# Optimization experiments

Measured on AMD Instinct MI355X. Metric: run time of the kernel, lower is better.

## Reference

```python
import jax, jax.numpy as jnp
import numpy as np

N_NODES = 50000
N_EDGES = 800000
IN_FEAT = 128
HIDDEN = 128
NUM_CLASS = 40


def setup_inputs() -> dict:
    key = jax.random.key(0)
    ks = jax.random.split(key, 8)
    feat = jax.random.normal(ks[0], (N_NODES, IN_FEAT), dtype=jnp.float32)
    # Glorot-ish init scale for reference weights
    W1 = jax.random.normal(ks[1], (IN_FEAT, HIDDEN), dtype=jnp.float32) / np.sqrt(IN_FEAT)
    b1 = jnp.zeros((HIDDEN,), dtype=jnp.float32)
    W2 = jax.random.normal(ks[2], (HIDDEN, HIDDEN), dtype=jnp.float32) / np.sqrt(HIDDEN)
    b2 = jnp.zeros((HIDDEN,), dtype=jnp.float32)
    W3 = jax.random.normal(ks[3], (HIDDEN, NUM_CLASS), dtype=jnp.float32) / np.sqrt(HIDDEN)
    b3 = jnp.zeros((NUM_CLASS,), dtype=jnp.float32)
    src = jax.random.randint(ks[4], (N_EDGES,), 0, N_NODES, dtype=jnp.int32)
    dst = jax.random.randint(ks[5], (N_EDGES,), 0, N_NODES, dtype=jnp.int32)
    return {"feat": feat, "W1": W1, "b1": b1, "W2": W2, "b2": b2,
            "W3": W3, "b3": b3, "src": src, "dst": dst}


def reference(feat, W1, b1, W2, b2, W3, b3, src, dst):
    # symmetric 'both' normalization as in DGL GraphConv:
    # h_dst = deg_in(dst)^{-1/2} * sum_{e:(s->d)} deg_out(s)^{-1/2} * (x_s W) + b
    ones = jnp.ones((src.shape[0],), dtype=feat.dtype)
    out_deg = jax.ops.segment_sum(ones, src, num_segments=N_NODES)
    in_deg = jax.ops.segment_sum(ones, dst, num_segments=N_NODES)
    out_norm = jax.lax.rsqrt(jnp.maximum(out_deg, 1.0))  # [N]
    in_norm = jax.lax.rsqrt(jnp.maximum(in_deg, 1.0))    # [N]

    def gconv(h, W, b):
        h = (h * out_norm[:, None]) @ W                  # [N, d_out]
        agg = jax.ops.segment_sum(h[src], dst, num_segments=N_NODES)
        return agg * in_norm[:, None] + b

    # eval mode: BatchNorm disabled (identity), dropout is a no-op
    h = jax.nn.relu(gconv(feat, W1, b1))
    h = jax.nn.relu(gconv(h, W2, b2))
    return gconv(h, W3, b3)
```

## Files before the change

### kernel.cpp

```cpp
#include <hip/hip_runtime.h>
#include <hip/hip_bf16.h>

#define N_NODES 50000
#define N_EDGES 800000
#define FEAT    128
#define HID     128
#define NCLS    40
#define XPAD    50048

#define RANGE   12500
#define NRANGE  4
#define NS      32
#define SLICE   (N_EDGES / NS)
#define NBLK    49

static constexpr size_t ALIGNB = 256;
static constexpr size_t aln(size_t x){ return (x + ALIGNB - 1) & ~(ALIGNB - 1); }
static constexpr size_t OFF_ONORM   = 0;
static constexpr size_t OFF_INORM   = OFF_ONORM + aln((size_t)N_NODES * 4);
static constexpr size_t OFF_ROWPTR  = OFF_INORM + aln((size_t)N_NODES * 4);
static constexpr size_t OFF_BSUM    = OFF_ROWPTR + aln((size_t)(N_NODES + 1) * 4);
static constexpr size_t OFF_BOFF    = OFF_BSUM + aln(64 * 4);
static constexpr size_t OFF_WT1     = OFF_BOFF + aln(64 * 4);
static constexpr size_t OFF_WT2     = OFF_WT1 + aln((size_t)128 * 128 * 2);
static constexpr size_t OFF_WT3     = OFF_WT2 + aln((size_t)128 * 128 * 2);
static constexpr size_t OFF_ESRC    = OFF_WT3 + aln((size_t)64 * 128 * 2);
static constexpr size_t OFF_HTMP    = OFF_ESRC + aln((size_t)N_EDGES * 4);
static constexpr size_t OFF_XBUF    = OFF_HTMP + aln((size_t)XPAD * 128 * 2);
static constexpr size_t OFF_PART    = OFF_HTMP;

__device__ __forceinline__ float bflo(unsigned u){
  union { unsigned i; float f; } c; c.i = u << 16; return c.f;
}
__device__ __forceinline__ float bfhi(unsigned u){
  union { unsigned i; float f; } c; c.i = u & 0xffff0000u; return c.f;
}
__device__ __forceinline__ unsigned pkbf(float a, float b){
  union { __hip_bfloat16 h; unsigned short u; } ca, cb;
  ca.h = __float2bfloat16(a); cb.h = __float2bfloat16(b);
  return ((unsigned)cb.u << 16) | (unsigned)ca.u;
}
__device__ __forceinline__ unsigned short bf1(float a){
  union { __hip_bfloat16 h; unsigned short u; } c;
  c.h = __float2bfloat16(a); return c.u;
}

typedef __attribute__((ext_vector_type(8))) short bf16x8;
typedef __attribute__((ext_vector_type(4))) float f32x4;

__global__ void k_prep_all(const float* __restrict__ W1, const float* __restrict__ W2,
                           const float* __restrict__ W3,
                           unsigned* __restrict__ wt1, unsigned* __restrict__ wt2,
                           unsigned* __restrict__ wt3){
  int b = blockIdx.x, t = threadIdx.x;
  const float* W; unsigned* Wt; int WC; int idx;
  if (b < 32)      { W = W1; Wt = wt1; WC = 128; idx = b * 256 + t; }
  else if (b < 64) { W = W2; Wt = wt2; WC = 128; idx = (b - 32) * 256 + t; }
  else             { W = W3; Wt = wt3; WC = 40;  idx = (b - 64) * 256 + t; }
  int c = idx >> 6, kp = idx & 63;
  float v0 = (c < WC) ? W[(size_t)(2 * kp)     * WC + c] : 0.f;
  float v1 = (c < WC) ? W[(size_t)(2 * kp + 1) * WC + c] : 0.f;
  Wt[idx] = pkbf(v0, v1);
}

__global__ __launch_bounds__(1024) void k_hist_lds(const int* __restrict__ src,
                                                   const int* __restrict__ dst,
                                                   unsigned* __restrict__ part){
  __shared__ unsigned h[RANGE];
  const int s = blockIdx.x, r = blockIdx.y, z = blockIdx.z;
  const int* __restrict__ idx = z ? src : dst;
  const int lo = r * RANGE;
  for (int i = threadIdx.x; i < RANGE; i += 1024) h[i] = 0;
  __syncthreads();
  const int e0 = s * SLICE;
  for (int e = e0 + threadIdx.x; e < e0 + SLICE; e += 1024){
    int v = idx[e] - lo;
    if ((unsigned)v < RANGE) atomicAdd(&h[v], 1u);
  }
  __syncthreads();
  unsigned* p = part + (((size_t)z * NRANGE + r) * NS + s) * RANGE;
  for (int i = threadIdx.x; i < RANGE; i += 1024) p[i] = h[i];
}

__global__ __launch_bounds__(1024) void k_scan1(const unsigned* __restrict__ part,
                                                int* __restrict__ rowptr,
                                                unsigned* __restrict__ bsum,
                                                float* __restrict__ inorm,
                                                float* __restrict__ onorm){
  __shared__ int wsum[16];
  const int t = threadIdx.x, lane = t & 63, w = t >> 6;
  const int i = blockIdx.x * 1024 + t;
  int v = 0;
  if (i < N_NODES){
    int r = i / RANGE, off = i % RANGE;
    const unsigned* pi = part + ((size_t)r * NS) * RANGE + off;
    const unsigned* po = part + (((size_t)NRANGE + r) * NS) * RANGE + off;
    unsigned si = 0, so = 0;
    #pragma unroll 8
    for (int s = 0; s < NS; ++s){
      si += pi[(size_t)s * RANGE];
      so += po[(size_t)s * RANGE];
    }
    inorm[i] = rsqrtf(fmaxf((float)si, 1.0f));
    onorm[i] = rsqrtf(fmaxf((float)so, 1.0f));
    v = (int)si;
  }
  int x = v;
  #pragma unroll
  for (int off = 1; off < 64; off <<= 1){
    int y = __shfl_up(x, off, 64);
    if (lane >= off) x += y;
  }
  if (lane == 63) wsum[w] = x;
  __syncthreads();
  if (w == 0 && lane < 16){
    int s = wsum[lane];
    #pragma unroll
    for (int off = 1; off < 16; off <<= 1){
      int y = __shfl_up(s, off, 64);
      if (lane >= off) s += y;
    }
    wsum[lane] = s;
  }
  __syncthreads();
  int woff = (w > 0) ? wsum[w - 1] : 0;
  if (i < N_NODES) rowptr[i] = woff + x - v;
  if (t == 0) bsum[blockIdx.x] = (unsigned)wsum[15];
}

__global__ void k_scan2(const unsigned* __restrict__ bsum, unsigned* __restrict__ boff){
  const int t = threadIdx.x;
  int v = (t < NBLK) ? (int)bsum[t] : 0;
  int x = v;
  #pragma unroll
  for (int off = 1; off < 64; off <<= 1){
    int y = __shfl_up(x, off, 64);
    if (t >= off) x += y;
  }
  if (t < NBLK) boff[t] = (unsigned)(x - v);
  if (t == NBLK - 1) boff[NBLK] = (unsigned)x;
}

__global__ __launch_bounds__(1024) void k_scan3(int* __restrict__ rowptr,
                                                const unsigned* __restrict__ boff,
                                                unsigned* __restrict__ part){
  const int i = blockIdx.x * 1024 + threadIdx.x;
  if (i < N_NODES){
    int rp = rowptr[i] + (int)boff[blockIdx.x];
    rowptr[i] = rp;
    int r = i / RANGE, off = i % RANGE;
    unsigned* p = part + ((size_t)r * NS) * RANGE + off;
    unsigned run = (unsigned)rp;
    #pragma unroll 8
    for (int s = 0; s < NS; ++s){
      unsigned c = p[(size_t)s * RANGE];
      p[(size_t)s * RANGE] = run;
      run += c;
    }
  } else if (i == N_NODES) rowptr[i] = (int)boff[NBLK];
}

__global__ __launch_bounds__(1024) void k_scatter_lds(const int* __restrict__ src,
                                                      const int* __restrict__ dst,
                                                      const unsigned* __restrict__ part,
                                                      int* __restrict__ esrc){
  __shared__ unsigned cur[RANGE];
  const int s = blockIdx.x, r = blockIdx.y;
  const int lo = r * RANGE;
  const unsigned* p = part + ((size_t)r * NS + s) * RANGE;
  for (int i = threadIdx.x; i < RANGE; i += 1024) cur[i] = p[i];
  __syncthreads();
  const int e0 = s * SLICE;
  for (int e = e0 + threadIdx.x; e < e0 + SLICE; e += 1024){
    int v = dst[e] - lo;
    if ((unsigned)v < RANGE){
      unsigned pos = atomicAdd(&cur[v], 1u);
      esrc[pos] = src[e];
    }
  }
}

template<int CT, int WCOUT, int OUTC, bool IN_F32>
__global__ __launch_bounds__(256) void k_gemm_mfma(const void* __restrict__ xin,
                                                   const unsigned short* __restrict__ wt,
                                                   const float* __restrict__ onorm,
                                                   unsigned short* __restrict__ outb){
  __shared__ unsigned short Wl[CT * 16][136];
  const int t = threadIdx.x;
  const int lane = t & 63;
  const int w = t >> 6;
  const int ln15 = lane & 15;
  const int quad = lane >> 4;

  {
    const uint4* w4 = (const uint4*)wt;
    #pragma unroll
    for (int i = 0; i < CT; ++i){
      int idx = t + i * 256;
      int row = idx >> 4, q = idx & 15;
      *(uint4*)&Wl[row][q * 8] = w4[idx];
    }
  }
  __syncthreads();

  f32x4 acc[CT];
  #pragma unroll
  for (int ct = 0; ct < CT; ++ct) acc[ct] = (f32x4){0.f, 0.f, 0.f, 0.f};

  const int xr = min(blockIdx.x * 64 + w * 16 + ln15, N_NODES - 1);
  #pragma unroll
  for (int kp = 0; kp < 4; ++kp){
    bf16x8 a;
    if (IN_F32){
      const float4* x4 = (const float4*)xin + (size_t)xr * 32;
      float4 p0 = x4[kp * 8 + quad * 2];
      float4 p1 = x4[kp * 8 + quad * 2 + 1];
      union { bf16x8 v; unsigned u[4]; } ua;
      ua.u[0] = pkbf(p0.x, p0.y); ua.u[1] = pkbf(p0.z, p0.w);
      ua.u[2] = pkbf(p1.x, p1.y); ua.u[3] = pkbf(p1.z, p1.w);
      a = ua.v;
    } else {
      const unsigned short* xrow = (const unsigned short*)xin + (size_t)xr * 128;
      a = *(const bf16x8*)(xrow + kp * 32 + quad * 8);
    }
    #pragma unroll
    for (int ct = 0; ct < CT; ++ct){
      bf16x8 b = *(const bf16x8*)&Wl[ct * 16 + ln15][kp * 32 + quad * 8];
      acc[ct] = __builtin_amdgcn_mfma_f32_16x16x32_bf16(a, b, acc[ct], 0, 0, 0);
    }
  }

  const int rowbase = blockIdx.x * 64 + w * 16 + quad * 4;
  float o[4];
  #pragma unroll
  for (int j = 0; j < 4; ++j){
    int r = rowbase + j;
    o[j] = (r < N_NODES) ? onorm[r] : 0.f;
  }
  #pragma unroll
  for (int ct = 0; ct < CT; ++ct){
    int col = ct * 16 + ln15;
    if (WCOUT < CT * 16 && col >= WCOUT) continue;
    #pragma unroll
    for (int j = 0; j < 4; ++j){
      int r = rowbase + j;
      if (r < N_NODES)
        outb[(size_t)r * OUTC + col] = bf1(acc[ct][j] * o[j]);
    }
  }
}

template<int CW, bool RELU, bool OUTBF>
__global__ __launch_bounds__(256) void k_agg(const unsigned* __restrict__ htmp,
                                             const int* __restrict__ rowptr,
                                             const int* __restrict__ esrc,
                                             const float* __restrict__ inorm,
                                             const float* __restrict__ bias,
                                             void* __restrict__ outv){
  constexpr int CU = CW / 2;
  const int wave = threadIdx.x >> 6;
  const int lane = threadIdx.x & 63;
  const int node = blockIdx.x * 4 + wave;
  if (node >= N_NODES) return;
  const int start = rowptr[node], end = rowptr[node + 1];
  float aL[4] = {0.f, 0.f, 0.f, 0.f};
  float aH[4] = {0.f, 0.f, 0.f, 0.f};
  for (int e0 = start; e0 < end; e0 += 64){
    const int n = min(64, end - e0);
    int el = (lane < n) ? esrc[e0 + lane] : 0;
    int j = 0;
    for (; j + 8 <= n; j += 8){
      int ss[8];
      #pragma unroll
      for (int q = 0; q < 8; ++q) ss[q] = __shfl(el, j + q);
      if (lane < CU){
        unsigned uu[8];
        #pragma unroll
        for (int q = 0; q < 8; ++q) uu[q] = htmp[(size_t)ss[q] * CU + lane];
        #pragma unroll
        for (int q = 0; q < 8; ++q){ aL[q & 3] += bflo(uu[q]); aH[q & 3] += bfhi(uu[q]); }
      }
    }
    for (; j + 4 <= n; j += 4){
      int ss[4];
      #pragma unroll
      for (int q = 0; q < 4; ++q) ss[q] = __shfl(el, j + q);
      if (lane < CU){
        unsigned uu[4];
        #pragma unroll
        for (int q = 0; q < 4; ++q) uu[q] = htmp[(size_t)ss[q] * CU + lane];
        #pragma unroll
        for (int q = 0; q < 4; ++q){ aL[q] += bflo(uu[q]); aH[q] += bfhi(uu[q]); }
      }
    }
    for (; j < n; ++j){
      int s0 = __shfl(el, j);
      if (lane < CU){
        unsigned u0 = htmp[(size_t)s0 * CU + lane];
        aL[0] += bflo(u0); aH[0] += bfhi(u0);
      }
    }
  }
  if (lane < CU){
    float sc = inorm[node];
    float y0 = ((aL[0] + aL[1]) + (aL[2] + aL[3])) * sc + bias[2 * lane];
    float y1 = ((aH[0] + aH[1]) + (aH[2] + aH[3])) * sc + bias[2 * lane + 1];
    if (RELU){ y0 = fmaxf(y0, 0.f); y1 = fmaxf(y1, 0.f); }
    if (OUTBF){
      ((unsigned*)outv)[(size_t)node * CU + lane] = pkbf(y0, y1);
    } else {
      float2 v; v.x = y0; v.y = y1;
      *(float2*)&((float*)outv)[(size_t)node * CW + 2 * lane] = v;
    }
  }
}

extern "C" void kernel_launch(void* const* d_in, const int* in_sizes, int n_in,
                              void* d_out, int out_size, void* d_ws, size_t ws_size,
                              hipStream_t stream){
  const float* feat = (const float*)d_in[0];
  const float* W1   = (const float*)d_in[1];
  const float* b1   = (const float*)d_in[2];
  const float* W2   = (const float*)d_in[3];
  const float* b2   = (const float*)d_in[4];
  const float* W3   = (const float*)d_in[5];
  const float* b3   = (const float*)d_in[6];
  const int* src = (const int*)d_in[7];
  const int* dst = (const int*)d_in[8];
  float* out = (float*)d_out;

  char* ws = (char*)d_ws;
  float*    onorm   = (float*)   (ws + OFF_ONORM);
  float*    inorm   = (float*)   (ws + OFF_INORM);
  int*      rowptr  = (int*)     (ws + OFF_ROWPTR);
  unsigned* bsum    = (unsigned*)(ws + OFF_BSUM);
  unsigned* boff    = (unsigned*)(ws + OFF_BOFF);
  unsigned* wt1     = (unsigned*)(ws + OFF_WT1);
  unsigned* wt2     = (unsigned*)(ws + OFF_WT2);
  unsigned* wt3     = (unsigned*)(ws + OFF_WT3);
  int*      esrc    = (int*)     (ws + OFF_ESRC);
  unsigned short* htmp = (unsigned short*)(ws + OFF_HTMP);
  unsigned short* xbuf = (unsigned short*)(ws + OFF_XBUF);
  unsigned* part    = (unsigned*)(ws + OFF_PART);

  k_prep_all    <<<80, 256, 0, stream>>>(W1, W2, W3, wt1, wt2, wt3);
  k_hist_lds    <<<dim3(NS, NRANGE, 2), 1024, 0, stream>>>(src, dst, part);
  k_scan1       <<<NBLK, 1024, 0, stream>>>(part, rowptr, bsum, inorm, onorm);
  k_scan2       <<<1, 64, 0, stream>>>(bsum, boff);
  k_scan3       <<<NBLK, 1024, 0, stream>>>(rowptr, boff, part);
  k_scatter_lds <<<dim3(NS, NRANGE), 1024, 0, stream>>>(src, dst, part, esrc);

  const int GB = XPAD / 64;
  const int AB = (N_NODES + 3) / 4;
  k_gemm_mfma<8, 128, 128, true ><<<GB, 256, 0, stream>>>(feat, (unsigned short*)wt1, onorm, htmp);
  k_agg<128, true, true ><<<AB, 256, 0, stream>>>((unsigned*)htmp, rowptr, esrc, inorm, b1, xbuf);
  k_gemm_mfma<8, 128, 128, false><<<GB, 256, 0, stream>>>(xbuf, (unsigned short*)wt2, onorm, htmp);
  k_agg<128, true, true ><<<AB, 256, 0, stream>>>((unsigned*)htmp, rowptr, esrc, inorm, b2, xbuf);
  k_gemm_mfma<4, 40, 40, false><<<GB, 256, 0, stream>>>(xbuf, (unsigned short*)wt3, onorm, htmp);
  k_agg<40, false, false><<<AB, 256, 0, stream>>>((unsigned*)htmp, rowptr, esrc, inorm, b3, out);
}
```

Baseline: 248.7 us.

## Fuse aggregation with following GEMM via LDS tile and fold weight prep into histogram

Layers 1 and 2 aggregation are fused with the next layer's MFMA GEMM. Each 512-thread block gathers 128 node rows, applies norm, bias and ReLU, and stages them as bf16 in LDS before multiplying by the next weight matrix. This removes the round trip of the intermediate xbuf through global memory and two kernel launches. The weight transpose/prep kernel is merged into the histogram kernel to save another launch. The cost is fewer blocks, since only 391 fused blocks run the irregular gather, and extra buffers to avoid aliasing.

New measurement: 267.3 us. 1.07x slower.

```diff
diff --git a/kernel.cpp b/kernel.cpp
--- a/kernel.cpp
+++ b/kernel.cpp
@@ -25,9 +25,10 @@
 static constexpr size_t OFF_WT2     = OFF_WT1 + aln((size_t)128 * 128 * 2);
 static constexpr size_t OFF_WT3     = OFF_WT2 + aln((size_t)128 * 128 * 2);
 static constexpr size_t OFF_ESRC    = OFF_WT3 + aln((size_t)64 * 128 * 2);
-static constexpr size_t OFF_HTMP    = OFF_ESRC + aln((size_t)N_EDGES * 4);
-static constexpr size_t OFF_XBUF    = OFF_HTMP + aln((size_t)XPAD * 128 * 2);
-static constexpr size_t OFF_PART    = OFF_HTMP;
+static constexpr size_t OFF_HTMPA   = OFF_ESRC + aln((size_t)N_EDGES * 4);
+static constexpr size_t OFF_HTMPB   = OFF_HTMPA + aln((size_t)XPAD * 128 * 2);
+static constexpr size_t OFF_HTMPC   = OFF_HTMPB + aln((size_t)XPAD * 128 * 2);
+static constexpr size_t OFF_PART    = OFF_HTMPA;
 
 __device__ __forceinline__ float bflo(unsigned u){
   union { unsigned i; float f; } c; c.i = u << 16; return c.f;
@@ -48,33 +49,35 @@
 typedef __attribute__((ext_vector_type(8))) short bf16x8;
 typedef __attribute__((ext_vector_type(4))) float f32x4;
 
-__global__ void k_prep_all(const float* __restrict__ W1, const float* __restrict__ W2,
-                           const float* __restrict__ W3,
-                           unsigned* __restrict__ wt1, unsigned* __restrict__ wt2,
-                           unsigned* __restrict__ wt3){
-  int b = blockIdx.x, t = threadIdx.x;
-  const float* W; unsigned* Wt; int WC; int idx;
-  if (b < 32)      { W = W1; Wt = wt1; WC = 128; idx = b * 256 + t; }
-  else if (b < 64) { W = W2; Wt = wt2; WC = 128; idx = (b - 32) * 256 + t; }
-  else             { W = W3; Wt = wt3; WC = 40;  idx = (b - 64) * 256 + t; }
-  int c = idx >> 6, kp = idx & 63;
-  float v0 = (c < WC) ? W[(size_t)(2 * kp)     * WC + c] : 0.f;
-  float v1 = (c < WC) ? W[(size_t)(2 * kp + 1) * WC + c] : 0.f;
-  Wt[idx] = pkbf(v0, v1);
-}
-
 __global__ __launch_bounds__(1024) void k_hist_lds(const int* __restrict__ src,
                                                    const int* __restrict__ dst,
-                                                   unsigned* __restrict__ part){
+                                                   unsigned* __restrict__ part,
+                                                   const float* __restrict__ W1,
+                                                   const float* __restrict__ W2,
+                                                   const float* __restrict__ W3,
+                                                   unsigned* __restrict__ wt1,
+                                                   unsigned* __restrict__ wt2,
+                                                   unsigned* __restrict__ wt3){
   __shared__ unsigned h[RANGE];
   const int s = blockIdx.x, r = blockIdx.y, z = blockIdx.z;
-  const int* __restrict__ idx = z ? src : dst;
+  if (z == 0 && r == 0 && s < 20){
+    int idx = s * 1024 + threadIdx.x;
+    const float* W; unsigned* Wt; int WC;
+    if (idx < 8192)       { W = W1; Wt = wt1; WC = 128; }
+    else if (idx < 16384) { W = W2; Wt = wt2; WC = 128; idx -= 8192; }
+    else                  { W = W3; Wt = wt3; WC = 40;  idx -= 16384; }
+    int c = idx >> 6, kp = idx & 63;
+    float v0 = (c < WC) ? W[(size_t)(2 * kp)     * WC + c] : 0.f;
+    float v1 = (c < WC) ? W[(size_t)(2 * kp + 1) * WC + c] : 0.f;
+    Wt[idx] = pkbf(v0, v1);
+  }
+  const int* __restrict__ idxp = z ? src : dst;
   const int lo = r * RANGE;
   for (int i = threadIdx.x; i < RANGE; i += 1024) h[i] = 0;
   __syncthreads();
   const int e0 = s * SLICE;
   for (int e = e0 + threadIdx.x; e < e0 + SLICE; e += 1024){
-    int v = idx[e] - lo;
+    int v = idxp[e] - lo;
     if ((unsigned)v < RANGE) atomicAdd(&h[v], 1u);
   }
   __syncthreads();
@@ -180,11 +183,76 @@
   }
 }
 
-template<int CT, int WCOUT, int OUTC, bool IN_F32>
-__global__ __launch_bounds__(256) void k_gemm_mfma(const void* __restrict__ xin,
-                                                   const unsigned short* __restrict__ wt,
-                                                   const float* __restrict__ onorm,
-                                                   unsigned short* __restrict__ outb){
+__global__ __launch_bounds__(256) void k_gemm1(const float* __restrict__ xin,
+                                               const unsigned short* __restrict__ wt,
+                                               const float* __restrict__ onorm,
+                                               unsigned short* __restrict__ outb){
+  __shared__ unsigned short Wl[128][136];
+  const int t = threadIdx.x;
+  const int lane = t & 63;
+  const int w = t >> 6;
+  const int ln15 = lane & 15;
+  const int quad = lane >> 4;
+  {
+    const uint4* w4 = (const uint4*)wt;
+    #pragma unroll
+    for (int i = 0; i < 8; ++i){
+      int idx = t + i * 256;
+      int row = idx >> 4, q = idx & 15;
+      *(uint4*)&Wl[row][q * 8] = w4[idx];
+    }
+  }
+  __syncthreads();
+
+  f32x4 acc[8];
+  #pragma unroll
+  for (int ct = 0; ct < 8; ++ct) acc[ct] = (f32x4){0.f, 0.f, 0.f, 0.f};
+
+  const int xr = min(blockIdx.x * 64 + w * 16 + ln15, N_NODES - 1);
+  #pragma unroll
+  for (int kp = 0; kp < 4; ++kp){
+    const float4* x4 = (const float4*)xin + (size_t)xr * 32;
+    float4 p0 = x4[kp * 8 + quad * 2];
+    float4 p1 = x4[kp * 8 + quad * 2 + 1];
+    union { bf16x8 v; unsigned u[4]; } ua;
+    ua.u[0] = pkbf(p0.x, p0.y); ua.u[1] = pkbf(p0.z, p0.w);
+    ua.u[2] = pkbf(p1.x, p1.y); ua.u[3] = pkbf(p1.z, p1.w);
+    bf16x8 a = ua.v;
+    #pragma unroll
+    for (int ct = 0; ct < 8; ++ct){
+      bf16x8 b = *(const bf16x8*)&Wl[ct * 16 + ln15][kp * 32 + quad * 8];
+      acc[ct] = __builtin_amdgcn_mfma_f32_16x16x32_bf16(a, b, acc[ct], 0, 0, 0);
+    }
+  }
+  const int rowbase = blockIdx.x * 64 + w * 16 + quad * 4;
+  float o[4];
+  #pragma unroll
+  for (int j = 0; j < 4; ++j){
+    int r = rowbase + j;
+    o[j] = (r < N_NODES) ? onorm[r] : 0.f;
+  }
+  #pragma unroll
+  for (int ct = 0; ct < 8; ++ct){
+    int col = ct * 16 + ln15;
+    #pragma unroll
+    for (int j = 0; j < 4; ++j){
+      int r = rowbase + j;
+      if (r < N_NODES)
+        outb[(size_t)r * 128 + col] = bf1(acc[ct][j] * o[j]);
+    }
+  }
+}
+
+template<int CT, int WCOUT, int OUTC>
+__global__ __launch_bounds__(512, 4) void k_agg_gemm(const unsigned* __restrict__ hin,
+                                                     const int* __restrict__ rowptr,
+                                                     const int* __restrict__ esrc,
+                                                     const float* __restrict__ inorm,
+                                                     const float* __restrict__ bias,
+                                                     const unsigned short* __restrict__ wt,
+                                                     const float* __restrict__ onorm,
+                                                     unsigned short* __restrict__ outb){
+  __shared__ unsigned short Xl[128][136];
   __shared__ unsigned short Wl[CT * 16][136];
   const int t = threadIdx.x;
   const int lane = t & 63;
@@ -195,42 +263,75 @@
   {
     const uint4* w4 = (const uint4*)wt;
     #pragma unroll
-    for (int i = 0; i < CT; ++i){
-      int idx = t + i * 256;
+    for (int i = 0; i < CT / 2; ++i){
+      int idx = t + i * 512;
       int row = idx >> 4, q = idx & 15;
       *(uint4*)&Wl[row][q * 8] = w4[idx];
     }
   }
+
+  const float b0 = bias[2 * lane], b1 = bias[2 * lane + 1];
+  const int rbase = blockIdx.x * 128 + w * 16;
+  for (int m = 0; m < 16; ++m){
+    const int g = rbase + m;
+    unsigned pk = 0u;
+    if (g < N_NODES){
+      const int start = rowptr[g], end = rowptr[g + 1];
+      float aL[4] = {0.f, 0.f, 0.f, 0.f};
+      float aH[4] = {0.f, 0.f, 0.f, 0.f};
+      for (int e0 = start; e0 < end; e0 += 64){
+        const int n = min(64, end - e0);
+        int el = (lane < n) ? esrc[e0 + lane] : 0;
+        int j = 0;
+        for (; j + 8 <= n; j += 8){
+          int ss[8];
+          #pragma unroll
+          for (int q = 0; q < 8; ++q) ss[q] = __shfl(el, j + q);
+          unsigned uu[8];
+          #pragma unroll
+          for (int q = 0; q < 8; ++q) uu[q] = hin[(size_t)ss[q] * 64 + lane];
+          #pragma unroll
+          for (int q = 0; q < 8; ++q){ aL[q & 3] += bflo(uu[q]); aH[q & 3] += bfhi(uu[q]); }
+        }
+        for (; j + 4 <= n; j += 4){
+          int ss[4];
+          #pragma unroll
+          for (int q = 0; q < 4; ++q) ss[q] = __shfl(el, j + q);
+          unsigned uu[4];
+          #pragma unroll
+          for (int q = 0; q < 4; ++q) uu[q] = hin[(size_t)ss[q] * 64 + lane];
+          #pragma unroll
+          for (int q = 0; q < 4; ++q){ aL[q] += bflo(uu[q]); aH[q] += bfhi(uu[q]); }
+        }
+        for (; j < n; ++j){
+          int s0 = __shfl(el, j);
+          unsigned u0 = hin[(size_t)s0 * 64 + lane];
+          aL[0] += bflo(u0); aH[0] += bfhi(u0);
+        }
+      }
+      float sc = inorm[g];
+      float y0 = ((aL[0] + aL[1]) + (aL[2] + aL[3])) * sc + b0;
+      float y1 = ((aH[0] + aH[1]) + (aH[2] + aH[3])) * sc + b1;
+      y0 = fmaxf(y0, 0.f); y1 = fmaxf(y1, 0.f);
+      pk = pkbf(y0, y1);
+    }
+    ((unsigned*)&Xl[w * 16 + m][0])[lane] = pk;
+  }
   __syncthreads();
 
   f32x4 acc[CT];
   #pragma unroll
   for (int ct = 0; ct < CT; ++ct) acc[ct] = (f32x4){0.f, 0.f, 0.f, 0.f};
-
-  const int xr = min(blockIdx.x * 64 + w * 16 + ln15, N_NODES - 1);
   #pragma unroll
   for (int kp = 0; kp < 4; ++kp){
-    bf16x8 a;
-    if (IN_F32){
-      const float4* x4 = (const float4*)xin + (size_t)xr * 32;
-      float4 p0 = x4[kp * 8 + quad * 2];
-      float4 p1 = x4[kp * 8 + quad * 2 + 1];
-      union { bf16x8 v; unsigned u[4]; } ua;
-      ua.u[0] = pkbf(p0.x, p0.y); ua.u[1] = pkbf(p0.z, p0.w);
-      ua.u[2] = pkbf(p1.x, p1.y); ua.u[3] = pkbf(p1.z, p1.w);
-      a = ua.v;
-    } else {
-      const unsigned short* xrow = (const unsigned short*)xin + (size_t)xr * 128;
-      a = *(const bf16x8*)(xrow + kp * 32 + quad * 8);
-    }
+    bf16x8 a = *(const bf16x8*)&Xl[w * 16 + ln15][kp * 32 + quad * 8];
     #pragma unroll
     for (int ct = 0; ct < CT; ++ct){
       bf16x8 b = *(const bf16x8*)&Wl[ct * 16 + ln15][kp * 32 + quad * 8];
       acc[ct] = __builtin_amdgcn_mfma_f32_16x16x32_bf16(a, b, acc[ct], 0, 0, 0);
     }
   }
-
-  const int rowbase = blockIdx.x * 64 + w * 16 + quad * 4;
+  const int rowbase = blockIdx.x * 128 + w * 16 + quad * 4;
   float o[4];
   #pragma unroll
   for (int j = 0; j < 4; ++j){
@@ -250,14 +351,13 @@
   }
 }
 
-template<int CW, bool RELU, bool OUTBF>
-__global__ __launch_bounds__(256) void k_agg(const unsigned* __restrict__ htmp,
-                                             const int* __restrict__ rowptr,
-                                             const int* __restrict__ esrc,
-                                             const float* __restrict__ inorm,
-                                             const float* __restrict__ bias,
-                                             void* __restrict__ outv){
-  constexpr int CU = CW / 2;
+__global__ __launch_bounds__(256) void k_agg3(const unsigned* __restrict__ htmp,
+                                              const int* __restrict__ rowptr,
+                                              const int* __restrict__ esrc,
+                                              const float* __restrict__ inorm,
+                                              const float* __restrict__ bias,
+                                              float* __restrict__ outf){
+  constexpr int CU = 20;
   const int wave = threadIdx.x >> 6;
   const int lane = threadIdx.x & 63;
   const int node = blockIdx.x * 4 + wave;
@@ -305,13 +405,8 @@
     float sc = inorm[node];
     float y0 = ((aL[0] + aL[1]) + (aL[2] + aL[3])) * sc + bias[2 * lane];
     float y1 = ((aH[0] + aH[1]) + (aH[2] + aH[3])) * sc + bias[2 * lane + 1];
-    if (RELU){ y0 = fmaxf(y0, 0.f); y1 = fmaxf(y1, 0.f); }
-    if (OUTBF){
-      ((unsigned*)outv)[(size_t)node * CU + lane] = pkbf(y0, y1);
-    } else {
-      float2 v; v.x = y0; v.y = y1;
-      *(float2*)&((float*)outv)[(size_t)node * CW + 2 * lane] = v;
-    }
+    float2 v; v.x = y0; v.y = y1;
+    *(float2*)&outf[(size_t)node * 40 + 2 * lane] = v;
   }
 }
 
@@ -339,23 +434,22 @@
   unsigned* wt2     = (unsigned*)(ws + OFF_WT2);
   unsigned* wt3     = (unsigned*)(ws + OFF_WT3);
   int*      esrc    = (int*)     (ws + OFF_ESRC);
-  unsigned short* htmp = (unsigned short*)(ws + OFF_HTMP);
-  unsigned short* xbuf = (unsigned short*)(ws + OFF_XBUF);
+  unsigned short* htmpA = (unsigned short*)(ws + OFF_HTMPA);
+  unsigned short* htmpB = (unsigned short*)(ws + OFF_HTMPB);
+  unsigned short* htmpC = (unsigned short*)(ws + OFF_HTMPC);
   unsigned* part    = (unsigned*)(ws + OFF_PART);
 
-  k_prep_all    <<<80, 256, 0, stream>>>(W1, W2, W3, wt1, wt2, wt3);
-  k_hist_lds    <<<dim3(NS, NRANGE, 2), 1024, 0, stream>>>(src, dst, part);
+  k_hist_lds    <<<dim3(NS, NRANGE, 2), 1024, 0, stream>>>(src, dst, part,
+                                                           W1, W2, W3, wt1, wt2, wt3);
   k_scan1       <<<NBLK, 1024, 0, stream>>>(part, rowptr, bsum, inorm, onorm);
   k_scan2       <<<1, 64, 0, stream>>>(bsum, boff);
   k_scan3       <<<NBLK, 1024, 0, stream>>>(rowptr, boff, part);
   k_scatter_lds <<<dim3(NS, NRANGE), 1024, 0, stream>>>(src, dst, part, esrc);
 
-  const int GB = XPAD / 64;
-  const int AB = (N_NODES + 3) / 4;
-  k_gemm_mfma<8, 128, 128, true ><<<GB, 256, 0, stream>>>(feat, (unsigned short*)wt1, onorm, htmp);
-  k_agg<128, true, true ><<<AB, 256, 0, stream>>>((unsigned*)htmp, rowptr, esrc, inorm, b1, xbuf);
-  k_gemm_mfma<8, 128, 128, false><<<GB, 256, 0, stream>>>(xbuf, (unsigned short*)wt2, onorm, htmp);
-  k_agg<128, true, true ><<<AB, 256, 0, stream>>>((unsigned*)htmp, rowptr, esrc, inorm, b2, xbuf);
-  k_gemm_mfma<4, 40, 40, false><<<GB, 256, 0, stream>>>(xbuf, (unsigned short*)wt3, onorm, htmp);
-  k_agg<40, false, false><<<AB, 256, 0, stream>>>((unsigned*)htmp, rowptr, esrc, inorm, b3, out);
-}
+  k_gemm1<<<XPAD / 64, 256, 0, stream>>>(feat, (unsigned short*)wt1, onorm, htmpA);
+  k_agg_gemm<8, 128, 128><<<XPAD / 128, 512, 0, stream>>>((unsigned*)htmpA, rowptr, esrc,
+                inorm, b1, (unsigned short*)wt2, onorm, htmpB);
+  k_agg_gemm<4, 40, 40><<<XPAD / 128, 512, 0, stream>>>((unsigned*)htmpB, rowptr, esrc,
+                inorm, b2, (unsigned short*)wt3, onorm, htmpC);
+  k_agg3<<<(N_NODES + 3) / 4, 256, 0, stream>>>((unsigned*)htmpC, rowptr, esrc, inorm, b3, out);
+}
```
